# Kernel optimization log

Measured on AMD Instinct MI355X. Metric: run time of the kernel, lower is better.

Reference implementation:

```python
import jax, jax.numpy as jnp
import numpy as np
import math

B, T, C, H = 2, 2048, 1024, 16
D = C // H  # head dim = 64


def setup_inputs() -> dict:
    key = jax.random.key(0)
    ks = jax.random.split(key, 9)
    s = 1.0 / math.sqrt(C)
    inp = {
        "x": jax.random.normal(ks[0], (B, T, C), dtype=jnp.float32),
        "Wk": jax.random.normal(ks[1], (C, C), dtype=jnp.float32) * s,
        "bk": jax.random.normal(ks[2], (C,), dtype=jnp.float32) * s,
        "Wq": jax.random.normal(ks[3], (C, C), dtype=jnp.float32) * s,
        "bq": jax.random.normal(ks[4], (C,), dtype=jnp.float32) * s,
        "Wv": jax.random.normal(ks[5], (C, C), dtype=jnp.float32) * s,
        "bv": jax.random.normal(ks[6], (C,), dtype=jnp.float32) * s,
        "Wo": jax.random.normal(ks[7], (C, C), dtype=jnp.float32) * s,
        "bo": jax.random.normal(ks[8], (C,), dtype=jnp.float32) * s,
    }
    return inp


def reference(x, Wk, bk, Wq, bq, Wv, bv, Wo, bo):
    # QKV projections, split heads: [B,T,C] -> [B,H,T,D]
    def proj(W, b):
        return (x @ W.T + b).reshape(B, T, H, D).transpose(0, 2, 1, 3)

    k = proj(Wk, bk)
    q = proj(Wq, bq)
    v = proj(Wv, bv)

    # NOTE: original scales by 1/sqrt(embedding_dim), not head_dim
    scale = 1.0 / math.sqrt(C)
    scores = jnp.einsum("bhtd,bhsd->bhts", q, k) * scale  # [B,H,T,T]
    causal = jnp.tril(jnp.ones((T, T), dtype=bool))
    scores = jnp.where(causal[None, None], scores, -jnp.inf)
    attn = jax.nn.softmax(scores, axis=-1)
    y = jnp.einsum("bhts,bhsd->bhtd", attn, v)  # [B,H,T,D]
    y = y.transpose(0, 2, 1, 3).reshape(B, T, C)
    return y @ Wo.T + bo
```

## Files before the change

kernel.cpp:

```cpp
#include <hip/hip_runtime.h>
#include <hip/hip_bf16.h>
#include <stdint.h>
#include <stddef.h>

#define B_ 2
#define T_ 2048
#define C_ 1024
#define H_ 16
#define D_ 64
#define M_ (B_*T_)

typedef __attribute__((ext_vector_type(8))) short short8;
typedef __attribute__((ext_vector_type(4))) float f32x4;
typedef __attribute__((ext_vector_type(16))) float f32x16;
typedef __attribute__((ext_vector_type(4))) unsigned int u32x4;

__device__ __forceinline__ unsigned short f2bf(float f) {
    unsigned u = __float_as_uint(f);
    unsigned r = 0x7FFFu + ((u >> 16) & 1u);
    return (unsigned short)((u + r) >> 16);
}

__device__ __forceinline__ unsigned cvtpk_bf16(float lo, float hi) {
    unsigned r;
    asm("v_cvt_pk_bf16_f32 %0, %1, %2" : "=v"(r) : "v"(lo), "v"(hi));
    return r;
}

__device__ __forceinline__ float fexp2(float x) {
    float r;
    asm("v_exp_f32 %0, %1" : "=v"(r) : "v"(x));
    return r;
}

__device__ __forceinline__ void plswap(unsigned &a, unsigned &b) {
    asm("v_permlane32_swap_b32 %0, %1" : "+v"(a), "+v"(b));
}

__device__ __forceinline__ float xhalf_max(float v) {
    float a = v, b = v;
    asm("" : "+v"(b));
    asm("v_permlane32_swap_b32 %0, %1" : "+v"(a), "+v"(b));
    return fmaxf(a, b);
}
__device__ __forceinline__ float xhalf_sum(float v) {
    float a = v, b = v;
    asm("" : "+v"(b));
    asm("v_permlane32_swap_b32 %0, %1" : "+v"(a), "+v"(b));
    return a + b;
}

__device__ __forceinline__ void gload16(const void* g, void* l) {
    __builtin_amdgcn_global_load_lds(
        (__attribute__((address_space(1))) void*)g,
        (__attribute__((address_space(3))) void*)l,
        16, 0, 0);
}

__global__ void cvt_bf16(const float* __restrict__ in,
                         unsigned short* __restrict__ out, int n) {
    int idx = (blockIdx.x * blockDim.x + threadIdx.x) * 4;
    if (idx >= n) return;
    float4 v = *reinterpret_cast<const float4*>(in + idx);
    ushort4 o;
    o.x = f2bf(v.x); o.y = f2bf(v.y); o.z = f2bf(v.z); o.w = f2bf(v.w);
    *reinterpret_cast<ushort4*>(out + idx) = o;
}

__global__ void cvt_bf16_w4(const float* __restrict__ a, const float* __restrict__ b,
                            const float* __restrict__ c, const float* __restrict__ d,
                            unsigned short* __restrict__ oa, unsigned short* __restrict__ ob,
                            unsigned short* __restrict__ oc, unsigned short* __restrict__ od,
                            int n) {
    int idx = (blockIdx.x * blockDim.x + threadIdx.x) * 4;
    if (idx >= n) return;
    const float* in = (blockIdx.y == 0) ? a : (blockIdx.y == 1) ? b : (blockIdx.y == 2) ? c : d;
    unsigned short* out = (blockIdx.y == 0) ? oa : (blockIdx.y == 1) ? ob : (blockIdx.y == 2) ? oc : od;
    float4 v = *reinterpret_cast<const float4*>(in + idx);
    ushort4 o;
    o.x = f2bf(v.x); o.y = f2bf(v.y); o.z = f2bf(v.z); o.w = f2bf(v.w);
    *reinterpret_cast<ushort4*>(out + idx) = o;
}

__global__ __launch_bounds__(256) void gemm_qkv(
    const unsigned short* __restrict__ A,
    const unsigned short* __restrict__ W0,
    const unsigned short* __restrict__ W1,
    const unsigned short* __restrict__ W2,
    const float* __restrict__ b0,
    const float* __restrict__ b1,
    const float* __restrict__ b2,
    unsigned short* __restrict__ o0,
    unsigned short* __restrict__ o1,
    unsigned short* __restrict__ o2)
{
    __shared__ unsigned short As[128*32];
    __shared__ unsigned short Bs[128*32];
    int which = blockIdx.x >> 8;
    int bx = blockIdx.x & 255;
    int bm = bx >> 3, bn = bx & 7;
    const unsigned short* W = (which==0) ? W0 : ((which==1) ? W1 : W2);
    const float* bias = (which==0) ? b0 : ((which==1) ? b1 : b2);

    int tid = threadIdx.x;
    int lane = tid & 63;
    int fr = lane & 15, fq = lane >> 4;
    int wid = tid >> 6;
    int wr = wid >> 1, wc = wid & 1;

    int srow = tid >> 2;
    int scol = (tid & 3) << 3;
    const unsigned short* Ab = A + (size_t)(bm*128 + srow) * C_ + scol;
    const unsigned short* Wb = W + (size_t)(bn*128 + srow) * C_ + scol;

    f32x4 acc[4][4] = {};

    for (int kt = 0; kt < C_/32; ++kt) {
        int ko = kt*32;
        gload16(Ab + ko,            &As[tid*8]);
        gload16(Ab + 64*C_ + ko,    &As[2048 + tid*8]);
        gload16(Wb + ko,            &Bs[tid*8]);
        gload16(Wb + 64*C_ + ko,    &Bs[2048 + tid*8]);
        __syncthreads();
        short8 af[4], bfr[4];
        #pragma unroll
        for (int i = 0; i < 4; ++i) {
            af[i]  = *reinterpret_cast<const short8*>(&As[(wr*64 + i*16 + fr)*32 + fq*8]);
            bfr[i] = *reinterpret_cast<const short8*>(&Bs[(wc*64 + i*16 + fr)*32 + fq*8]);
        }
        #pragma unroll
        for (int i = 0; i < 4; ++i)
            #pragma unroll
            for (int j = 0; j < 4; ++j)
                acc[i][j] = __builtin_amdgcn_mfma_f32_16x16x32_bf16(af[i], bfr[j], acc[i][j], 0, 0, 0);
        __syncthreads();
    }

    float sc = (which == 1) ? 0.045084220f : 1.0f;
    int mbase = bm*128 + wr*64;
    int nbase = bn*128 + wc*64;
    #pragma unroll
    for (int j = 0; j < 4; ++j) {
        int col = nbase + j*16 + fr;
        float bv = bias[col];
        int h = col >> 6, d = col & 63;
        #pragma unroll
        for (int i = 0; i < 4; ++i) {
            int r0 = mbase + i*16 + fq*4;
            #pragma unroll
            for (int r = 0; r < 4; ++r) {
                float v = (acc[i][j][r] + bv) * sc;
                int m = r0 + r;
                int b = m >> 11, t = m & (T_-1);
                unsigned short hv = f2bf(v);
                if (which == 2)
                    o2[((size_t)(b*H_ + h)*D_ + d)*T_ + t] = hv;
                else {
                    unsigned short* o = (which==0) ? o0 : o1;
                    o[((size_t)(b*H_ + h)*T_ + t)*D_ + d] = hv;
                }
            }
        }
    }
}

__global__ __launch_bounds__(256) void gemm_out(
    const unsigned short* __restrict__ A,
    const unsigned short* __restrict__ W,
    const float* __restrict__ bias,
    float* __restrict__ out)
{
    __shared__ unsigned short As[128*32];
    __shared__ unsigned short Bs[128*32];
    int bx = blockIdx.x;
    int bm = bx >> 3, bn = bx & 7;

    int tid = threadIdx.x;
    int lane = tid & 63;
    int fr = lane & 15, fq = lane >> 4;
    int wid = tid >> 6;
    int wr = wid >> 1, wc = wid & 1;

    int srow = tid >> 2;
    int scol = (tid & 3) << 3;
    const unsigned short* Ab = A + (size_t)(bm*128 + srow) * C_ + scol;
    const unsigned short* Wb = W + (size_t)(bn*128 + srow) * C_ + scol;

    f32x4 acc[4][4] = {};

    for (int kt = 0; kt < C_/32; ++kt) {
        int ko = kt*32;
        gload16(Ab + ko,            &As[tid*8]);
        gload16(Ab + 64*C_ + ko,    &As[2048 + tid*8]);
        gload16(Wb + ko,            &Bs[tid*8]);
        gload16(Wb + 64*C_ + ko,    &Bs[2048 + tid*8]);
        __syncthreads();
        short8 af[4], bfr[4];
        #pragma unroll
        for (int i = 0; i < 4; ++i) {
            af[i]  = *reinterpret_cast<const short8*>(&As[(wr*64 + i*16 + fr)*32 + fq*8]);
            bfr[i] = *reinterpret_cast<const short8*>(&Bs[(wc*64 + i*16 + fr)*32 + fq*8]);
        }
        #pragma unroll
        for (int i = 0; i < 4; ++i)
            #pragma unroll
            for (int j = 0; j < 4; ++j)
                acc[i][j] = __builtin_amdgcn_mfma_f32_16x16x32_bf16(af[i], bfr[j], acc[i][j], 0, 0, 0);
        __syncthreads();
    }

    int mbase = bm*128 + wr*64;
    int nbase = bn*128 + wc*64;
    #pragma unroll
    for (int j = 0; j < 4; ++j) {
        int col = nbase + j*16 + fr;
        float bv = bias[col];
        #pragma unroll
        for (int i = 0; i < 4; ++i) {
            int r0 = mbase + i*16 + fq*4;
            #pragma unroll
            for (int r = 0; r < 4; ++r)
                out[(size_t)(r0 + r)*C_ + col] = acc[i][j][r] + bv;
        }
    }
}

__device__ __forceinline__ void attn_subtile(
    const short8 (&kf)[4], const short8 (&qf)[4],
    const short8 (&vlo)[2], const short8 (&vhi)[2],
    bool diag, int l31, int hi,
    f32x16& o0, f32x16& o1, float& m_, float& l_)
{
    f32x16 a0 = {};
    __builtin_amdgcn_s_setprio(1);
    a0 = __builtin_amdgcn_mfma_f32_32x32x16_bf16(kf[0], qf[0], a0, 0, 0, 0);
    a0 = __builtin_amdgcn_mfma_f32_32x32x16_bf16(kf[1], qf[1], a0, 0, 0, 0);
    a0 = __builtin_amdgcn_mfma_f32_32x32x16_bf16(kf[2], qf[2], a0, 0, 0, 0);
    a0 = __builtin_amdgcn_mfma_f32_32x32x16_bf16(kf[3], qf[3], a0, 0, 0, 0);
    __builtin_amdgcn_s_setprio(0);

    if (diag) {
        #pragma unroll
        for (int r = 0; r < 16; ++r) {
            int kvl = (r&3) + 8*(r>>2) + 4*hi;
            if (kvl > l31) a0[r] = -1e30f;
        }
    }

    float x0 = fmaxf(a0[0], a0[1]),   x1 = fmaxf(a0[2], a0[3]);
    float x2 = fmaxf(a0[4], a0[5]),   x3 = fmaxf(a0[6], a0[7]);
    float x4 = fmaxf(a0[8], a0[9]),   x5 = fmaxf(a0[10], a0[11]);
    float x6 = fmaxf(a0[12], a0[13]), x7 = fmaxf(a0[14], a0[15]);
    float y0 = fmaxf(x0, x1), y1 = fmaxf(x2, x3), y2 = fmaxf(x4, x5), y3 = fmaxf(x6, x7);
    float pm = fmaxf(fmaxf(y0, y1), fmaxf(y2, y3));
    pm = xhalf_max(pm);

    if (!__all(pm - m_ <= 8.0f)) {
        float mn = fmaxf(m_, pm);
        float alpha = fexp2(m_ - mn);
        l_ *= alpha;
        m_ = mn;
        #pragma unroll
        for (int r = 0; r < 16; ++r) {
            int row = (r&3) + 8*(r>>2) + 4*hi;
            float ar = __shfl(alpha, row);
            o0[r] *= ar;
            o1[r] *= ar;
        }
    }

    #pragma unroll
    for (int r = 0; r < 16; ++r)
        a0[r] = fexp2(a0[r] - m_);
    float s0 = a0[0]+a0[1],  s1 = a0[2]+a0[3],  s2 = a0[4]+a0[5],   s3 = a0[6]+a0[7];
    float s4 = a0[8]+a0[9],  s5 = a0[10]+a0[11], s6 = a0[12]+a0[13], s7 = a0[14]+a0[15];
    float u0 = s0+s1, u1 = s2+s3, u2 = s4+s5, u3 = s6+s7;
    float rs = (u0+u1) + (u2+u3);
    rs = xhalf_sum(rs);
    l_ += rs;

    unsigned pk_[8];
    #pragma unroll
    for (int jj = 0; jj < 8; ++jj)
        pk_[jj] = cvtpk_bf16(a0[2*jj], a0[2*jj+1]);

    #pragma unroll
    for (int kb = 0; kb < 2; ++kb) {
        unsigned fx = pk_[4*kb+0], fz = pk_[4*kb+2];
        unsigned fy = pk_[4*kb+1], fw = pk_[4*kb+3];
        plswap(fx, fz);
        plswap(fy, fw);
        u32x4 wv;
        wv.x = fx; wv.y = fy; wv.z = fz; wv.w = fw;
        short8 pfrag = __builtin_bit_cast(short8, wv);
        __builtin_amdgcn_s_setprio(1);
        o0 = __builtin_amdgcn_mfma_f32_32x32x16_bf16(pfrag, vlo[kb], o0, 0, 0, 0);
        o1 = __builtin_amdgcn_mfma_f32_32x32x16_bf16(pfrag, vhi[kb], o1, 0, 0, 0);
        __builtin_amdgcn_s_setprio(0);
    }
}

__global__ __launch_bounds__(256, 2) void flash_attn(
    const unsigned short* __restrict__ q,
    const unsigned short* __restrict__ k,
    const unsigned short* __restrict__ vt,
    unsigned short* __restrict__ y)
{
    __shared__ __align__(16) unsigned short ST[2][4][4096];
    float* oP  = reinterpret_cast<float*>(&ST[0][0][0]);
    float* mlP = oP + 4*32*68;

    int tid = threadIdx.x, lane = tid & 63, w = tid >> 6;
    int l31 = lane & 31, hi = lane >> 5, rsw = l31 & 7;
    int role = w >> 1, pair = w & 1;
    int bid = blockIdx.x;

    int half = bid >> 8;
    int idx  = bid & 255;
    int bh   = (idx & 7)*4 + ((idx >> 3) & 3);
    int sidx = idx >> 5;
    int S    = half ? sidx : (15 - sidx);

    const unsigned short* kp = k  + (size_t)bh*T_*D_;
    const unsigned short* vp = vt + (size_t)bh*D_*T_;

    int rowbase = S*128 + pair*64;
    const unsigned short* qp = q + ((size_t)bh*T_ + rowbase) * D_;

    short8 qf0[4], qf1[4];
    #pragma unroll
    for (int dk = 0; dk < 4; ++dk) {
        qf0[dk] = *reinterpret_cast<const short8*>(qp + (size_t)l31*D_        + dk*16 + hi*8);
        qf1[dk] = *reinterpret_cast<const short8*>(qp + (size_t)(32 + l31)*D_ + dk*16 + hi*8);
    }

    f32x16 o00 = {}, o01 = {}, o10 = {}, o11 = {};
    float m0 = -1e30f, l0 = 0.f, m1 = -1e30f, l1 = 0.f;

    int lim0 = 4*S + 2*pair;
    int lim1 = lim0 + 1;
    int niter = S + 1;

    #define STAGE(ii, bufi)                                                            \
    {                                                                                  \
        _Pragma("unroll")                                                              \
        for (int jj = 0; jj < 2; ++jj) {                                               \
            int c2 = tid + jj*256;                                                     \
            int row_ = c2 >> 3;                                                        \
            int slot_ = (c2 & 7) ^ (row_ & 7);                                         \
            int tl_ = (ii), th_ = S + 1 + (ii);                                        \
            gload16(kp + ((size_t)(tl_*64 + row_))*D_ + slot_*8, &ST[bufi][0][c2*8]);  \
            gload16(kp + ((size_t)(th_*64 + row_))*D_ + slot_*8, &ST[bufi][1][c2*8]);  \
            gload16(vp + (size_t)row_*T_ + tl_*64 + slot_*8,     &ST[bufi][2][c2*8]);  \
            gload16(vp + (size_t)row_*T_ + th_*64 + slot_*8,     &ST[bufi][3][c2*8]);  \
        }                                                                              \
    }

    STAGE(0, 0);
    __syncthreads();

    for (int i = 0; i < niter; ++i) {
        int bufi = i & 1;
        if (i + 1 < niter) STAGE(i + 1, bufi ^ 1);

        const unsigned short* Kl = &ST[bufi][role][0];
        const unsigned short* Vl = &ST[bufi][2 + role][0];
        int t = role ? (S + 1 + i) : i;

        #pragma unroll
        for (int st = 0; st < 2; ++st) {
            int g = 2*t + st;
            if (g <= lim1) {
                short8 kf[4];
                const unsigned short* kr = Kl + (st*32 + l31)*64;
                #pragma unroll
                for (int dk = 0; dk < 4; ++dk)
                    kf[dk] = *reinterpret_cast<const short8*>(kr + (((dk<<1)|hi) ^ rsw)*8);
                short8 vlo[2], vhi[2];
                const unsigned short* vr0 = Vl + l31*64;
                const unsigned short* vr1 = Vl + (32 + l31)*64;
                #pragma unroll
                for (int kb = 0; kb < 2; ++kb) {
                    int sl = (((st<<2) | (kb<<1) | hi) ^ rsw) * 8;
                    vlo[kb] = *reinterpret_cast<const short8*>(vr0 + sl);
                    vhi[kb] = *reinterpret_cast<const short8*>(vr1 + sl);
                }
                if (g <= lim0)
                    attn_subtile(kf, qf0, vlo, vhi, g == lim0, l31, hi, o00, o01, m0, l0);
                attn_subtile(kf, qf1, vlo, vhi, g == lim1, l31, hi, o10, o11, m1, l1);
            }
        }
        __syncthreads();
    }
    #undef STAGE

    if (!role) {
        int s0 = pair*2, s1 = pair*2 + 1;
        #pragma unroll
        for (int rr = 0; rr < 16; ++rr) {
            int crow = (rr&3) + 8*(rr>>2) + 4*hi;
            oP[(s0*32 + crow)*68 + l31]      = o00[rr];
            oP[(s0*32 + crow)*68 + 32 + l31] = o01[rr];
            oP[(s1*32 + crow)*68 + l31]      = o10[rr];
            oP[(s1*32 + crow)*68 + 32 + l31] = o11[rr];
        }
        if (!hi) {
            mlP[s0*32 + l31]       = m0;
            mlP[128 + s0*32 + l31] = l0;
            mlP[s1*32 + l31]       = m1;
            mlP[128 + s1*32 + l31] = l1;
        }
    }
    __syncthreads();
    if (role) {
        int b = bh >> 4, h = bh & 15;
        #pragma unroll
        for (int qq = 0; qq < 2; ++qq) {
            int set = pair*2 + qq;
            const f32x16& po0 = qq ? o10 : o00;
            const f32x16& po1 = qq ? o11 : o01;
            float m_ = qq ? m1 : m0;
            float l_ = qq ? l1 : l0;

            float mA = mlP[set*32 + l31];
            float lA = mlP[128 + set*32 + l31];
            float mN = fmaxf(mA, m_);
            float aA = fexp2(mA - mN);
            float aB = fexp2(m_ - mN);
            float lN = lA*aA + l_*aB;
            float inv = 1.0f / lN;
            float cA = aA * inv, cB = aB * inv;

            #pragma unroll
            for (int rr = 0; rr < 16; ++rr) {
                int crow = (rr&3) + 8*(rr>>2) + 4*hi;
                float cAr = __shfl(cA, crow);
                float cBr = __shfl(cB, crow);
                float vA0 = oP[(set*32 + crow)*68 + l31];
                float vA1 = oP[(set*32 + crow)*68 + 32 + l31];
                int trow = rowbase + qq*32 + crow;
                size_t base = ((size_t)(b*T_ + trow))*C_ + h*64;
                y[base + l31]      = f2bf(vA0*cAr + po0[rr]*cBr);
                y[base + 32 + l31] = f2bf(vA1*cAr + po1[rr]*cBr);
            }
        }
    }
}

extern "C" void kernel_launch(void* const* d_in, const int* in_sizes, int n_in,
                              void* d_out, int out_size, void* d_ws, size_t ws_size,
                              hipStream_t stream) {
    const float* x  = (const float*)d_in[0];
    const float* Wk = (const float*)d_in[1];
    const float* bk = (const float*)d_in[2];
    const float* Wq = (const float*)d_in[3];
    const float* bq = (const float*)d_in[4];
    const float* Wv = (const float*)d_in[5];
    const float* bv = (const float*)d_in[6];
    const float* Wo = (const float*)d_in[7];
    const float* bo = (const float*)d_in[8];
    float* out = (float*)d_out;

    char* ws = (char*)d_ws;
    unsigned short* xb  = (unsigned short*)(ws);
    unsigned short* wkb = (unsigned short*)(ws + ((size_t)8  << 20));
    unsigned short* wqb = (unsigned short*)(ws + ((size_t)10 << 20));
    unsigned short* wvb = (unsigned short*)(ws + ((size_t)12 << 20));
    unsigned short* wob = (unsigned short*)(ws + ((size_t)14 << 20));
    unsigned short* qb  = (unsigned short*)(ws + ((size_t)16 << 20));
    unsigned short* kb  = (unsigned short*)(ws + ((size_t)24 << 20));
    unsigned short* vtb = (unsigned short*)(ws + ((size_t)32 << 20));
    unsigned short* yb  = (unsigned short*)(ws + ((size_t)40 << 20));

    const int nx = B_*T_*C_;
    const int nw = C_*C_;

    cvt_bf16<<<dim3(nx/4/256), dim3(256), 0, stream>>>(x, xb, nx);
    cvt_bf16_w4<<<dim3(nw/4/256, 4), dim3(256), 0, stream>>>(
        Wk, Wq, Wv, Wo, wkb, wqb, wvb, wob, nw);

    gemm_qkv<<<dim3(768), dim3(256), 0, stream>>>(xb, wkb, wqb, wvb, bk, bq, bv, kb, qb, vtb);

    flash_attn<<<dim3(512), dim3(256), 0, stream>>>(qb, kb, vtb, yb);

    gemm_out<<<dim3(256), dim3(256), 0, stream>>>(yb, wob, bo, out);
}
```

Baseline: 115.2 us.

## Interleave two query subtiles in attention and merge conversion kernels

The attention inner step now handles both query subtiles in one call. Their QK MFMAs are interleaved across four independent accumulators, the causal mask becomes branchless arithmetic, and the softmax and PV work for the two subtiles is fused, so dependent MFMA chains are shorter and there is more ILP. The fp32-to-bf16 conversion of x and the four weights is also merged into a single launch to save one kernel launch. The cost is higher register pressure, plus masked exp and MFMA work on subtiles that were skipped before when g > lim0, with the initial max changed to -1e29 so fully masked rows stay finite.

Result: slower. 117.7 us (+2.2%).

```diff
diff --git a/kernel.cpp b/kernel.cpp
--- a/kernel.cpp
+++ b/kernel.cpp
@@ -57,29 +57,23 @@
         16, 0, 0);
 }
 
-__global__ void cvt_bf16(const float* __restrict__ in,
-                         unsigned short* __restrict__ out, int n) {
+__global__ void cvt_all(const float* __restrict__ x,  const float* __restrict__ wk,
+                        const float* __restrict__ wq, const float* __restrict__ wv,
+                        const float* __restrict__ wo,
+                        unsigned short* __restrict__ xb,  unsigned short* __restrict__ wkb,
+                        unsigned short* __restrict__ wqb, unsigned short* __restrict__ wvb,
+                        unsigned short* __restrict__ wob) {
     int idx = (blockIdx.x * blockDim.x + threadIdx.x) * 4;
-    if (idx >= n) return;
-    float4 v = *reinterpret_cast<const float4*>(in + idx);
+    const float* in; unsigned short* out; int off;
+    if      (idx < (4<<20)) { in = x;  out = xb;  off = idx; }
+    else if (idx < (5<<20)) { in = wk; out = wkb; off = idx - (4<<20); }
+    else if (idx < (6<<20)) { in = wq; out = wqb; off = idx - (5<<20); }
+    else if (idx < (7<<20)) { in = wv; out = wvb; off = idx - (6<<20); }
+    else                    { in = wo; out = wob; off = idx - (7<<20); }
+    float4 v = *reinterpret_cast<const float4*>(in + off);
     ushort4 o;
     o.x = f2bf(v.x); o.y = f2bf(v.y); o.z = f2bf(v.z); o.w = f2bf(v.w);
-    *reinterpret_cast<ushort4*>(out + idx) = o;
-}
-
-__global__ void cvt_bf16_w4(const float* __restrict__ a, const float* __restrict__ b,
-                            const float* __restrict__ c, const float* __restrict__ d,
-                            unsigned short* __restrict__ oa, unsigned short* __restrict__ ob,
-                            unsigned short* __restrict__ oc, unsigned short* __restrict__ od,
-                            int n) {
-    int idx = (blockIdx.x * blockDim.x + threadIdx.x) * 4;
-    if (idx >= n) return;
-    const float* in = (blockIdx.y == 0) ? a : (blockIdx.y == 1) ? b : (blockIdx.y == 2) ? c : d;
-    unsigned short* out = (blockIdx.y == 0) ? oa : (blockIdx.y == 1) ? ob : (blockIdx.y == 2) ? oc : od;
-    float4 v = *reinterpret_cast<const float4*>(in + idx);
-    ushort4 o;
-    o.x = f2bf(v.x); o.y = f2bf(v.y); o.z = f2bf(v.z); o.w = f2bf(v.w);
-    *reinterpret_cast<ushort4*>(out + idx) = o;
+    *reinterpret_cast<ushort4*>(out + off) = o;
 }
 
 __global__ __launch_bounds__(256) void gemm_qkv(
@@ -225,77 +219,109 @@
     }
 }
 
-__device__ __forceinline__ void attn_subtile(
-    const short8 (&kf)[4], const short8 (&qf)[4],
+__device__ __forceinline__ void attn_subtile2(
+    const short8 (&kf)[4], const short8 (&qf0)[4], const short8 (&qf1)[4],
     const short8 (&vlo)[2], const short8 (&vhi)[2],
-    bool diag, int l31, int hi,
-    f32x16& o0, f32x16& o1, float& m_, float& l_)
+    int dg0, int l31, int hi,
+    f32x16& o00, f32x16& o01, float& m0, float& l0,
+    f32x16& o10, f32x16& o11, float& m1, float& l1)
 {
-    f32x16 a0 = {};
+    int dg1 = dg0 - 32;
+
+    f32x16 aA = {}, aB = {}, bA = {}, bB = {};
     __builtin_amdgcn_s_setprio(1);
-    a0 = __builtin_amdgcn_mfma_f32_32x32x16_bf16(kf[0], qf[0], a0, 0, 0, 0);
-    a0 = __builtin_amdgcn_mfma_f32_32x32x16_bf16(kf[1], qf[1], a0, 0, 0, 0);
-    a0 = __builtin_amdgcn_mfma_f32_32x32x16_bf16(kf[2], qf[2], a0, 0, 0, 0);
-    a0 = __builtin_amdgcn_mfma_f32_32x32x16_bf16(kf[3], qf[3], a0, 0, 0, 0);
+    aA = __builtin_amdgcn_mfma_f32_32x32x16_bf16(kf[0], qf0[0], aA, 0, 0, 0);
+    bA = __builtin_amdgcn_mfma_f32_32x32x16_bf16(kf[0], qf1[0], bA, 0, 0, 0);
+    aB = __builtin_amdgcn_mfma_f32_32x32x16_bf16(kf[1], qf0[1], aB, 0, 0, 0);
+    bB = __builtin_amdgcn_mfma_f32_32x32x16_bf16(kf[1], qf1[1], bB, 0, 0, 0);
+    aA = __builtin_amdgcn_mfma_f32_32x32x16_bf16(kf[2], qf0[2], aA, 0, 0, 0);
+    bA = __builtin_amdgcn_mfma_f32_32x32x16_bf16(kf[2], qf1[2], bA, 0, 0, 0);
+    aB = __builtin_amdgcn_mfma_f32_32x32x16_bf16(kf[3], qf0[3], aB, 0, 0, 0);
+    bB = __builtin_amdgcn_mfma_f32_32x32x16_bf16(kf[3], qf1[3], bB, 0, 0, 0);
     __builtin_amdgcn_s_setprio(0);
 
-    if (diag) {
-        #pragma unroll
-        for (int r = 0; r < 16; ++r) {
-            int kvl = (r&3) + 8*(r>>2) + 4*hi;
-            if (kvl > l31) a0[r] = -1e30f;
-        }
-    }
-
-    float x0 = fmaxf(a0[0], a0[1]),   x1 = fmaxf(a0[2], a0[3]);
-    float x2 = fmaxf(a0[4], a0[5]),   x3 = fmaxf(a0[6], a0[7]);
-    float x4 = fmaxf(a0[8], a0[9]),   x5 = fmaxf(a0[10], a0[11]);
-    float x6 = fmaxf(a0[12], a0[13]), x7 = fmaxf(a0[14], a0[15]);
-    float y0 = fmaxf(x0, x1), y1 = fmaxf(x2, x3), y2 = fmaxf(x4, x5), y3 = fmaxf(x6, x7);
-    float pm = fmaxf(fmaxf(y0, y1), fmaxf(y2, y3));
-    pm = xhalf_max(pm);
-
-    if (!__all(pm - m_ <= 8.0f)) {
-        float mn = fmaxf(m_, pm);
-        float alpha = fexp2(m_ - mn);
-        l_ *= alpha;
-        m_ = mn;
+    #pragma unroll
+    for (int r = 0; r < 16; ++r) {
+        int kvl = (r&3) + 8*(r>>2) + 4*hi;
+        int thr = l31 - kvl;
+        float v0 = aA[r] + aB[r];
+        float v1 = bA[r] + bB[r];
+        aA[r] = (dg0 > thr) ? -1e30f : v0;
+        bA[r] = (dg1 > thr) ? -1e30f : v1;
+    }
+
+    float p0a = fmaxf(aA[0], aA[1]),   p0b = fmaxf(aA[2], aA[3]);
+    float p0c = fmaxf(aA[4], aA[5]),   p0d = fmaxf(aA[6], aA[7]);
+    float p0e = fmaxf(aA[8], aA[9]),   p0f = fmaxf(aA[10], aA[11]);
+    float p0g = fmaxf(aA[12], aA[13]), p0h = fmaxf(aA[14], aA[15]);
+    float pm0 = fmaxf(fmaxf(fmaxf(p0a, p0b), fmaxf(p0c, p0d)),
+                      fmaxf(fmaxf(p0e, p0f), fmaxf(p0g, p0h)));
+    float p1a = fmaxf(bA[0], bA[1]),   p1b = fmaxf(bA[2], bA[3]);
+    float p1c = fmaxf(bA[4], bA[5]),   p1d = fmaxf(bA[6], bA[7]);
+    float p1e = fmaxf(bA[8], bA[9]),   p1f = fmaxf(bA[10], bA[11]);
+    float p1g = fmaxf(bA[12], bA[13]), p1h = fmaxf(bA[14], bA[15]);
+    float pm1 = fmaxf(fmaxf(fmaxf(p1a, p1b), fmaxf(p1c, p1d)),
+                      fmaxf(fmaxf(p1e, p1f), fmaxf(p1g, p1h)));
+    pm0 = xhalf_max(pm0);
+    pm1 = xhalf_max(pm1);
+
+    if (!__all((pm0 - m0 <= 8.0f) && (pm1 - m1 <= 8.0f))) {
+        float mn0 = fmaxf(m0, pm0);
+        float mn1 = fmaxf(m1, pm1);
+        float al0 = fexp2(m0 - mn0);
+        float al1 = fexp2(m1 - mn1);
+        l0 *= al0; m0 = mn0;
+        l1 *= al1; m1 = mn1;
         #pragma unroll
         for (int r = 0; r < 16; ++r) {
             int row = (r&3) + 8*(r>>2) + 4*hi;
-            float ar = __shfl(alpha, row);
-            o0[r] *= ar;
-            o1[r] *= ar;
-        }
-    }
-
-    #pragma unroll
-    for (int r = 0; r < 16; ++r)
-        a0[r] = fexp2(a0[r] - m_);
-    float s0 = a0[0]+a0[1],  s1 = a0[2]+a0[3],  s2 = a0[4]+a0[5],   s3 = a0[6]+a0[7];
-    float s4 = a0[8]+a0[9],  s5 = a0[10]+a0[11], s6 = a0[12]+a0[13], s7 = a0[14]+a0[15];
-    float u0 = s0+s1, u1 = s2+s3, u2 = s4+s5, u3 = s6+s7;
-    float rs = (u0+u1) + (u2+u3);
-    rs = xhalf_sum(rs);
-    l_ += rs;
-
-    unsigned pk_[8];
-    #pragma unroll
-    for (int jj = 0; jj < 8; ++jj)
-        pk_[jj] = cvtpk_bf16(a0[2*jj], a0[2*jj+1]);
+            float a0r = __shfl(al0, row);
+            float a1r = __shfl(al1, row);
+            o00[r] *= a0r; o01[r] *= a0r;
+            o10[r] *= a1r; o11[r] *= a1r;
+        }
+    }
+
+    #pragma unroll
+    for (int r = 0; r < 16; ++r) {
+        aA[r] = fexp2(aA[r] - m0);
+        bA[r] = fexp2(bA[r] - m1);
+    }
+    float s0a = aA[0]+aA[1],  s0b = aA[2]+aA[3],  s0c = aA[4]+aA[5],   s0d = aA[6]+aA[7];
+    float s0e = aA[8]+aA[9],  s0f = aA[10]+aA[11], s0g = aA[12]+aA[13], s0h = aA[14]+aA[15];
+    float rs0 = ((s0a+s0b) + (s0c+s0d)) + ((s0e+s0f) + (s0g+s0h));
+    float s1a = bA[0]+bA[1],  s1b = bA[2]+bA[3],  s1c = bA[4]+bA[5],   s1d = bA[6]+bA[7];
+    float s1e = bA[8]+bA[9],  s1f = bA[10]+bA[11], s1g = bA[12]+bA[13], s1h = bA[14]+bA[15];
+    float rs1 = ((s1a+s1b) + (s1c+s1d)) + ((s1e+s1f) + (s1g+s1h));
+    rs0 = xhalf_sum(rs0);
+    rs1 = xhalf_sum(rs1);
+    l0 += rs0;
+    l1 += rs1;
+
+    unsigned pk0[8], pk1[8];
+    #pragma unroll
+    for (int jj = 0; jj < 8; ++jj) {
+        pk0[jj] = cvtpk_bf16(aA[2*jj], aA[2*jj+1]);
+        pk1[jj] = cvtpk_bf16(bA[2*jj], bA[2*jj+1]);
+    }
 
     #pragma unroll
     for (int kb = 0; kb < 2; ++kb) {
-        unsigned fx = pk_[4*kb+0], fz = pk_[4*kb+2];
-        unsigned fy = pk_[4*kb+1], fw = pk_[4*kb+3];
-        plswap(fx, fz);
-        plswap(fy, fw);
-        u32x4 wv;
-        wv.x = fx; wv.y = fy; wv.z = fz; wv.w = fw;
-        short8 pfrag = __builtin_bit_cast(short8, wv);
+        unsigned f0x = pk0[4*kb+0], f0z = pk0[4*kb+2];
+        unsigned f0y = pk0[4*kb+1], f0w = pk0[4*kb+3];
+        plswap(f0x, f0z); plswap(f0y, f0w);
+        u32x4 w0; w0.x = f0x; w0.y = f0y; w0.z = f0z; w0.w = f0w;
+        short8 pf0 = __builtin_bit_cast(short8, w0);
+        unsigned f1x = pk1[4*kb+0], f1z = pk1[4*kb+2];
+        unsigned f1y = pk1[4*kb+1], f1w = pk1[4*kb+3];
+        plswap(f1x, f1z); plswap(f1y, f1w);
+        u32x4 w1; w1.x = f1x; w1.y = f1y; w1.z = f1z; w1.w = f1w;
+        short8 pf1 = __builtin_bit_cast(short8, w1);
         __builtin_amdgcn_s_setprio(1);
-        o0 = __builtin_amdgcn_mfma_f32_32x32x16_bf16(pfrag, vlo[kb], o0, 0, 0, 0);
-        o1 = __builtin_amdgcn_mfma_f32_32x32x16_bf16(pfrag, vhi[kb], o1, 0, 0, 0);
+        o00 = __builtin_amdgcn_mfma_f32_32x32x16_bf16(pf0, vlo[kb], o00, 0, 0, 0);
+        o10 = __builtin_amdgcn_mfma_f32_32x32x16_bf16(pf1, vlo[kb], o10, 0, 0, 0);
+        o01 = __builtin_amdgcn_mfma_f32_32x32x16_bf16(pf0, vhi[kb], o01, 0, 0, 0);
+        o11 = __builtin_amdgcn_mfma_f32_32x32x16_bf16(pf1, vhi[kb], o11, 0, 0, 0);
         __builtin_amdgcn_s_setprio(0);
     }
 }
@@ -335,7 +361,7 @@
     }
 
     f32x16 o00 = {}, o01 = {}, o10 = {}, o11 = {};
-    float m0 = -1e30f, l0 = 0.f, m1 = -1e30f, l1 = 0.f;
+    float m0 = -1e29f, l0 = 0.f, m1 = -1e29f, l1 = 0.f;
 
     int lim0 = 4*S + 2*pair;
     int lim1 = lim0 + 1;
@@ -385,9 +411,9 @@
                     vlo[kb] = *reinterpret_cast<const short8*>(vr0 + sl);
                     vhi[kb] = *reinterpret_cast<const short8*>(vr1 + sl);
                 }
-                if (g <= lim0)
-                    attn_subtile(kf, qf0, vlo, vhi, g == lim0, l31, hi, o00, o01, m0, l0);
-                attn_subtile(kf, qf1, vlo, vhi, g == lim1, l31, hi, o10, o11, m1, l1);
+                int dg0 = (g - lim0) << 5;
+                attn_subtile2(kf, qf0, qf1, vlo, vhi, dg0, l31, hi,
+                              o00, o01, m0, l0, o10, o11, m1, l1);
             }
         }
         __syncthreads();
@@ -472,12 +498,8 @@
     unsigned short* vtb = (unsigned short*)(ws + ((size_t)32 << 20));
     unsigned short* yb  = (unsigned short*)(ws + ((size_t)40 << 20));
 
-    const int nx = B_*T_*C_;
-    const int nw = C_*C_;
-
-    cvt_bf16<<<dim3(nx/4/256), dim3(256), 0, stream>>>(x, xb, nx);
-    cvt_bf16_w4<<<dim3(nw/4/256, 4), dim3(256), 0, stream>>>(
-        Wk, Wq, Wv, Wo, wkb, wqb, wvb, wob, nw);
+    cvt_all<<<dim3(8192), dim3(256), 0, stream>>>(
+        x, Wk, Wq, Wv, Wo, xb, wkb, wqb, wvb, wob);
 
     gemm_qkv<<<dim3(768), dim3(256), 0, stream>>>(xb, wkb, wqb, wvb, bk, bq, bv, kb, qb, vtb);
 
```
